# Optimization experiments

Measured on AMD Instinct MI355X. Metric: run time of the kernel, lower is better.

## Reference

```python
import jax, jax.numpy as jnp
import numpy as np

B, N, D_IN, D_H, D_OUT = 2, 512, 128, 128, 128


def _mlp2(x, W1, b1, W2, b2):
    # Linear -> SiLU -> Linear
    h = jax.nn.silu(x @ W1 + b1)
    return h @ W2 + b2


def _safe_norm(d2):
    # norm with zero (not NaN) gradient at 0, matching torch.norm's subgradient
    pos = d2 > 0
    return jnp.where(pos, jnp.sqrt(jnp.where(pos, d2, 1.0)), 0.0)


def setup_inputs() -> dict:
    key = jax.random.key(0)
    ks = jax.random.split(key, 16)

    def lin(k, fan_in, fan_out):
        bound = 1.0 / np.sqrt(fan_in)
        kw, kb = jax.random.split(k)
        W = jax.random.uniform(kw, (fan_in, fan_out), jnp.float32, -bound, bound)
        b = jax.random.uniform(kb, (fan_out,), jnp.float32, -bound, bound)
        return W, b

    Ws1, bs1 = lin(ks[0], D_IN, D_H)
    Ws2, bs2 = lin(ks[1], D_H, D_OUT)
    Wv1, bv1 = lin(ks[2], D_IN, D_H)
    Wv2, bv2 = lin(ks[3], D_H, D_OUT)
    Wa1, ba1 = lin(ks[4], D_IN + 3, D_H)
    Wa2, ba2 = lin(ks[5], D_H, 1)

    node_features = jax.random.normal(ks[6], (B, N, D_IN), jnp.float32)
    coordinates = jax.random.normal(ks[7], (B, N, 3), jnp.float32)
    edge_mask = jax.random.randint(ks[8], (B, N, N), 0, 2, jnp.int32)

    return dict(node_features=node_features, coordinates=coordinates, edge_mask=edge_mask,
                Ws1=Ws1, bs1=bs1, Ws2=Ws2, bs2=bs2,
                Wv1=Wv1, bv1=bv1, Wv2=Wv2, bv2=bv2,
                Wa1=Wa1, ba1=ba1, Wa2=Wa2, ba2=ba2)


def reference(node_features, coordinates, edge_mask,
              Ws1, bs1, Ws2, bs2, Wv1, bv1, Wv2, bv2, Wa1, ba1, Wa2, ba2):
    num_atoms = node_features.shape[1]

    # pairwise geometry: diff[b,i,j,:] = x_i - x_j
    diff = coordinates[:, :, None, :] - coordinates[:, None, :, :]  # [B,N,N,3]
    d2 = jnp.sum(diff * diff, axis=-1)
    distances = _safe_norm(d2)  # [B,N,N]

    # per-node scalar branch
    scalar_features = _mlp2(node_features, Ws1, bs1, Ws2, bs2)  # [B,N,D_OUT]

    # radial features + broadcast node features -> attention MLP
    dist_features = jnp.stack(
        [distances, 1.0 / (distances + 1e-6), jnp.exp(-distances)], axis=-1)  # [B,N,N,3]
    nf_exp = jnp.broadcast_to(node_features[:, :, None, :],
                              node_features.shape[:2] + (num_atoms, node_features.shape[-1]))
    attention_input = jnp.concatenate([nf_exp, dist_features], axis=-1)  # [B,N,N,D_IN+3]
    attn_logits = _mlp2(attention_input, Wa1, ba1, Wa2, ba2)[..., 0]  # [B,N,N]

    attn_logits = jnp.where(edge_mask != 0, attn_logits, -jnp.inf)
    attention_weights = jax.nn.softmax(attn_logits, axis=-1)  # [B,N,N]

    # direction-weighted aggregation
    vector_aggregated = jnp.einsum('bijc,bij->bic', diff, attention_weights)  # [B,N,3]

    vector_features = _mlp2(node_features, Wv1, bv1, Wv2, bv2)  # [B,N,D_OUT]
    vector_out = vector_aggregated * vector_features[..., :3]  # [B,N,3]

    return scalar_features, vector_out
```

## Files before the change

### kernel.cpp

```cpp
#include <hip/hip_runtime.h>
#include <math.h>

#define NB 2
#define NN 512
#define DD 128
#define LOG2E 1.4426950408889634f

typedef unsigned long long ull;

__device__ __forceinline__ float exp2_hw(float x) {
    float r; asm("v_exp_f32 %0, %1" : "=v"(r) : "v"(x)); return r;
}
__device__ __forceinline__ float silu_f(float x) {
    float e = exp2_hw(-LOG2E * x);
    return x * __builtin_amdgcn_rcpf(1.0f + e);
}

#define UPD(Wq, bbv, s)                                                        \
    { float pre = fmaf(f3[s], Wq.z, fmaf(f2[s], Wq.y, fmaf(f1[s], Wq.x, bbv))); \
      float e   = exp2_hw(pre);                                                \
      float rc  = __builtin_amdgcn_rcpf(1.0f + e);                             \
      acc[s]    = fmaf(pre * Wq.w, rc, acc[s]); }

__global__ __launch_bounds__(256) void k_all(
    const float* __restrict__ nf,
    const float* __restrict__ coords,
    const int*   __restrict__ mask,
    const float* __restrict__ Ws1, const float* __restrict__ bs1,
    const float* __restrict__ Ws2, const float* __restrict__ bs2,
    const float* __restrict__ Wv1, const float* __restrict__ bv1,
    const float* __restrict__ Wv2, const float* __restrict__ bv2,
    const float* __restrict__ Wa1, const float* __restrict__ ba1,
    const float* __restrict__ Wa2, const float* __restrict__ ba2p,
    float* __restrict__ scalar_out,
    float* __restrict__ vec_out)
{
    __shared__ __align__(16) float  s_nf[2][DD];
    __shared__ __align__(16) float  s_hs[2][DD];
    __shared__ __align__(16) float  s_hv[2][DD];
    __shared__ __align__(16) float  s_bb[2][DD];
    __shared__ __align__(16) float4 s_w4[DD];
    __shared__ float  s_part[3][2][256];
    __shared__ short  s_act[2][NN];
    __shared__ int    s_cnt8[2][8], s_off8[2][8], s_nact[2];
    __shared__ float  s_red[2][4], s_red2[2][4][4];

    const int row0 = blockIdx.x * 2;
    const int b    = row0 >> 9;
    const int tid  = threadIdx.x;
    const int lane = tid & 63;
    const int wid  = tid >> 6;
    const int c    = tid & 127;
    const int h    = tid >> 7;

    { const int rr = tid >> 7, t = tid & 127;
      s_nf[rr][t] = nf[(row0 + rr) * DD + t]; }

    const int* mrow0 = mask + (size_t)row0 * NN;
    const int* mrow1 = mrow0 + NN;
    const bool m00 = (mrow0[tid] != 0), m01 = (mrow0[tid + 256] != 0);
    const bool m10 = (mrow1[tid] != 0), m11 = (mrow1[tid + 256] != 0);
    const ull  b00 = __ballot(m00), b01 = __ballot(m01);
    const ull  b10 = __ballot(m10), b11 = __ballot(m11);
    if (lane == 0) {
        s_cnt8[0][wid]     = __popcll(b00);
        s_cnt8[0][4 + wid] = __popcll(b01);
        s_cnt8[1][wid]     = __popcll(b10);
        s_cnt8[1][4 + wid] = __popcll(b11);
    }
    __syncthreads();

    if (tid < 2) {
        int a = 0;
        #pragma unroll
        for (int q = 0; q < 8; ++q) { s_off8[tid][q] = a; a += s_cnt8[tid][q]; }
        s_nact[tid] = a;
    }

    {
        float pS0 = 0.f, pS1 = 0.f, pV0 = 0.f, pV1 = 0.f, pA0 = 0.f, pA1 = 0.f;
        const float4* nfq0 = (const float4*)s_nf[0];
        const float4* nfq1 = (const float4*)s_nf[1];
        const int kq0 = h * 16;
        #pragma unroll 4
        for (int kk = 0; kk < 16; ++kk) {
            float4 x0 = nfq0[kq0 + kk];
            float4 x1 = nfq1[kq0 + kk];
            const int k = (kq0 + kk) * 4;
            float w;
            w = Ws1[(k+0)*DD + c]; pS0 = fmaf(x0.x, w, pS0); pS1 = fmaf(x1.x, w, pS1);
            w = Ws1[(k+1)*DD + c]; pS0 = fmaf(x0.y, w, pS0); pS1 = fmaf(x1.y, w, pS1);
            w = Ws1[(k+2)*DD + c]; pS0 = fmaf(x0.z, w, pS0); pS1 = fmaf(x1.z, w, pS1);
            w = Ws1[(k+3)*DD + c]; pS0 = fmaf(x0.w, w, pS0); pS1 = fmaf(x1.w, w, pS1);
            w = Wv1[(k+0)*DD + c]; pV0 = fmaf(x0.x, w, pV0); pV1 = fmaf(x1.x, w, pV1);
            w = Wv1[(k+1)*DD + c]; pV0 = fmaf(x0.y, w, pV0); pV1 = fmaf(x1.y, w, pV1);
            w = Wv1[(k+2)*DD + c]; pV0 = fmaf(x0.z, w, pV0); pV1 = fmaf(x1.z, w, pV1);
            w = Wv1[(k+3)*DD + c]; pV0 = fmaf(x0.w, w, pV0); pV1 = fmaf(x1.w, w, pV1);
            w = Wa1[(k+0)*DD + c]; pA0 = fmaf(x0.x, w, pA0); pA1 = fmaf(x1.x, w, pA1);
            w = Wa1[(k+1)*DD + c]; pA0 = fmaf(x0.y, w, pA0); pA1 = fmaf(x1.y, w, pA1);
            w = Wa1[(k+2)*DD + c]; pA0 = fmaf(x0.z, w, pA0); pA1 = fmaf(x1.z, w, pA1);
            w = Wa1[(k+3)*DD + c]; pA0 = fmaf(x0.w, w, pA0); pA1 = fmaf(x1.w, w, pA1);
        }
        s_part[0][0][tid] = pS0; s_part[0][1][tid] = pS1;
        s_part[1][0][tid] = pV0; s_part[1][1][tid] = pV1;
        s_part[2][0][tid] = pA0; s_part[2][1][tid] = pA1;
    }
    __syncthreads();

    {
        const int rr = tid >> 7, t = tid & 127;
        s_hs[rr][t] = silu_f(s_part[0][rr][t] + s_part[0][rr][128 + t] + bs1[t]);
        s_hv[rr][t] = silu_f(s_part[1][rr][t] + s_part[1][rr][128 + t] + bv1[t]);
        s_bb[rr][t] = -LOG2E * (s_part[2][rr][t] + s_part[2][rr][128 + t] + ba1[t]);
    }
    if (tid < DD) {
        float4 w;
        w.x = -LOG2E * Wa1[128 * DD + tid];
        w.y = -LOG2E * Wa1[129 * DD + tid];
        w.z = -LOG2E * Wa1[130 * DD + tid];
        w.w = -Wa2[tid];
        s_w4[tid] = w;
    }
    {
        const ull lm = (1ull << lane) - 1ull;
        if (m00) s_act[0][s_off8[0][wid]     + __popcll(b00 & lm)] = (short)tid;
        if (m01) s_act[0][s_off8[0][4 + wid] + __popcll(b01 & lm)] = (short)(tid + 256);
        if (m10) s_act[1][s_off8[1][wid]     + __popcll(b10 & lm)] = (short)tid;
        if (m11) s_act[1][s_off8[1][4 + wid] + __popcll(b11 & lm)] = (short)(tid + 256);
    }
    __syncthreads();

    {
        float p0 = 0.f, p1 = 0.f;
        const float4* h0 = (const float4*)s_hs[0];
        const float4* h1 = (const float4*)s_hs[1];
        const int kq0 = h * 16;
        #pragma unroll 4
        for (int kk = 0; kk < 16; ++kk) {
            float4 x0 = h0[kq0 + kk];
            float4 x1 = h1[kq0 + kk];
            const int k = (kq0 + kk) * 4;
            float w;
            w = Ws2[(k+0)*DD + c]; p0 = fmaf(x0.x, w, p0); p1 = fmaf(x1.x, w, p1);
            w = Ws2[(k+1)*DD + c]; p0 = fmaf(x0.y, w, p0); p1 = fmaf(x1.y, w, p1);
            w = Ws2[(k+2)*DD + c]; p0 = fmaf(x0.z, w, p0); p1 = fmaf(x1.z, w, p1);
            w = Ws2[(k+3)*DD + c]; p0 = fmaf(x0.w, w, p0); p1 = fmaf(x1.w, w, p1);
        }
        s_part[0][0][tid] = p0; s_part[0][1][tid] = p1;
    }
    float* vfp = &s_part[1][0][0];
    if (tid < 192) {
        const int rr  = tid / 96;
        const int rem = tid % 96;
        const int col = rem >> 5;
        const int kq  = rem & 31;
        float vp = 0.f;
        #pragma unroll
        for (int u = 0; u < 4; ++u) {
            const int k = 4 * kq + u;
            vp = fmaf(s_hv[rr][k], Wv2[k * DD + col], vp);
        }
        vfp[tid] = vp;
    }

    const int n0 = __builtin_amdgcn_readfirstlane(s_nact[0]);
    const int n1 = __builtin_amdgcn_readfirstlane(s_nact[1]);
    const int wb = (tid & ~63) + 256;
    const bool has1r0 = wb < n0;
    const bool has1r1 = wb < n1;
    bool act[4];
    act[0] = tid < n0;  act[1] = tid + 256 < n0;
    act[2] = tid < n1;  act[3] = tid + 256 < n1;

    const float ba2l = ba2p[0] * LOG2E;
    float xi[2][3];
    #pragma unroll
    for (int rr = 0; rr < 2; ++rr)
        #pragma unroll
        for (int cc = 0; cc < 3; ++cc) xi[rr][cc] = coords[(row0 + rr) * 3 + cc];
    const float* cb = coords + (size_t)b * NN * 3;

    float dx[4], dy[4], dz[4], f1[4], f2[4], f3[4], acc[4];
    #pragma unroll
    for (int s = 0; s < 4; ++s) {
        acc[s] = ba2l;
        dx[s] = dy[s] = dz[s] = f1[s] = f2[s] = f3[s] = 0.f;
    }
    #pragma unroll
    for (int s = 0; s < 4; ++s) {
        const int rr = s >> 1;
        const bool rnd1 = (s & 1);
        if (rnd1 && !(rr == 0 ? has1r0 : has1r1)) continue;
        const int a = tid + (rnd1 ? 256 : 0);
        const int j = ((int)s_act[rr][act[s] ? a : 0]) & (NN - 1);
        dx[s] = xi[rr][0] - cb[j * 3 + 0];
        dy[s] = xi[rr][1] - cb[j * 3 + 1];
        dz[s] = xi[rr][2] - cb[j * 3 + 2];
        float d2 = fmaf(dx[s], dx[s], fmaf(dy[s], dy[s], dz[s] * dz[s]));
        float d  = sqrtf(d2);
        f1[s] = d;
        float x  = d + 1e-6f;
        float rc = __builtin_amdgcn_rcpf(x);
        f2[s] = rc * fmaf(-x, rc, 2.0f);
        f3[s] = exp2_hw(-LOG2E * d);
    }

    const float4* bbq0 = (const float4*)s_bb[0];
    const float4* bbq1 = (const float4*)s_bb[1];
    for (int t4 = 0; t4 < DD / 4; ++t4) {
        float4 W0 = s_w4[4 * t4 + 0];
        float4 W1 = s_w4[4 * t4 + 1];
        float4 W2 = s_w4[4 * t4 + 2];
        float4 W3 = s_w4[4 * t4 + 3];
        float4 bA = bbq0[t4];
        float4 bB = bbq1[t4];
        UPD(W0, bA.x, 0); UPD(W1, bA.y, 0); UPD(W2, bA.z, 0); UPD(W3, bA.w, 0);
        UPD(W0, bB.x, 2); UPD(W1, bB.y, 2); UPD(W2, bB.z, 2); UPD(W3, bB.w, 2);
        if (has1r0) {
            UPD(W0, bA.x, 1); UPD(W1, bA.y, 1); UPD(W2, bA.z, 1); UPD(W3, bA.w, 1);
        }
        if (has1r1) {
            UPD(W0, bB.x, 3); UPD(W1, bB.y, 3); UPD(W2, bB.z, 3); UPD(W3, bB.w, 3);
        }
    }
    __syncthreads();

    {
        const int rr = tid >> 7, t = tid & 127;
        scalar_out[(row0 + rr) * DD + t] =
            s_part[0][rr][t] + s_part[0][rr][128 + t] + bs2[t];
    }

    float mloc[2] = { -__builtin_inff(), -__builtin_inff() };
    if (act[0]) mloc[0] = acc[0];
    if (has1r0 && act[1]) mloc[0] = fmaxf(mloc[0], acc[1]);
    if (act[2]) mloc[1] = acc[2];
    if (has1r1 && act[3]) mloc[1] = fmaxf(mloc[1], acc[3]);
    #pragma unroll
    for (int ofs = 32; ofs >= 1; ofs >>= 1) {
        mloc[0] = fmaxf(mloc[0], __shfl_xor(mloc[0], ofs));
        mloc[1] = fmaxf(mloc[1], __shfl_xor(mloc[1], ofs));
    }
    if (lane == 0) { s_red[0][wid] = mloc[0]; s_red[1][wid] = mloc[1]; }
    __syncthreads();
    const float mx0 = fmaxf(fmaxf(s_red[0][0], s_red[0][1]), fmaxf(s_red[0][2], s_red[0][3]));
    const float mx1 = fmaxf(fmaxf(s_red[1][0], s_red[1][1]), fmaxf(s_red[1][2], s_red[1][3]));

    float es[2] = {0.f, 0.f}, wx[2] = {0.f, 0.f}, wy[2] = {0.f, 0.f}, wz[2] = {0.f, 0.f};
    if (act[0]) {
        float e = exp2_hw(acc[0] - mx0);
        es[0] += e; wx[0] = fmaf(e, dx[0], wx[0]); wy[0] = fmaf(e, dy[0], wy[0]); wz[0] = fmaf(e, dz[0], wz[0]);
    }
    if (has1r0 && act[1]) {
        float e = exp2_hw(acc[1] - mx0);
        es[0] += e; wx[0] = fmaf(e, dx[1], wx[0]); wy[0] = fmaf(e, dy[1], wy[0]); wz[0] = fmaf(e, dz[1], wz[0]);
    }
    if (act[2]) {
        float e = exp2_hw(acc[2] - mx1);
        es[1] += e; wx[1] = fmaf(e, dx[2], wx[1]); wy[1] = fmaf(e, dy[2], wy[1]); wz[1] = fmaf(e, dz[2], wz[1]);
    }
    if (has1r1 && act[3]) {
        float e = exp2_hw(acc[3] - mx1);
        es[1] += e; wx[1] = fmaf(e, dx[3], wx[1]); wy[1] = fmaf(e, dy[3], wy[1]); wz[1] = fmaf(e, dz[3], wz[1]);
    }
    #pragma unroll
    for (int ofs = 32; ofs >= 1; ofs >>= 1) {
        #pragma unroll
        for (int rr = 0; rr < 2; ++rr) {
            es[rr] += __shfl_xor(es[rr], ofs);
            wx[rr] += __shfl_xor(wx[rr], ofs);
            wy[rr] += __shfl_xor(wy[rr], ofs);
            wz[rr] += __shfl_xor(wz[rr], ofs);
        }
    }
    if (lane == 0) {
        #pragma unroll
        for (int rr = 0; rr < 2; ++rr) {
            s_red2[rr][wid][0] = es[rr]; s_red2[rr][wid][1] = wx[rr];
            s_red2[rr][wid][2] = wy[rr]; s_red2[rr][wid][3] = wz[rr];
        }
    }
    __syncthreads();

    if (tid < 6) {
        const int rr = tid / 3, cc = tid % 3;
        float tot = s_red2[rr][0][0] + s_red2[rr][1][0] + s_red2[rr][2][0] + s_red2[rr][3][0];
        float num = s_red2[rr][0][1+cc] + s_red2[rr][1][1+cc] + s_red2[rr][2][1+cc] + s_red2[rr][3][1+cc];
        float vf = bv2[cc];
        const float* pp = &vfp[rr * 96 + cc * 32];
        #pragma unroll 8
        for (int q = 0; q < 32; ++q) vf += pp[q];
        vec_out[(row0 + rr) * 3 + cc] = (num / tot) * vf;
    }
}

extern "C" void kernel_launch(void* const* d_in, const int* in_sizes, int n_in,
                              void* d_out, int out_size, void* d_ws, size_t ws_size,
                              hipStream_t stream) {
    const float* nf     = (const float*)d_in[0];
    const float* coords = (const float*)d_in[1];
    const int*   mask   = (const int*)  d_in[2];
    const float* Ws1 = (const float*)d_in[3];  const float* bs1 = (const float*)d_in[4];
    const float* Ws2 = (const float*)d_in[5];  const float* bs2 = (const float*)d_in[6];
    const float* Wv1 = (const float*)d_in[7];  const float* bv1 = (const float*)d_in[8];
    const float* Wv2 = (const float*)d_in[9];  const float* bv2 = (const float*)d_in[10];
    const float* Wa1 = (const float*)d_in[11]; const float* ba1 = (const float*)d_in[12];
    const float* Wa2 = (const float*)d_in[13]; const float* ba2 = (const float*)d_in[14];

    float* scalar_out = (float*)d_out;
    float* vec_out    = (float*)d_out + NB * NN * DD;

    hipLaunchKernelGGL(k_all, dim3(NB * NN / 2), dim3(256), 0, stream,
                       nf, coords, mask,
                       Ws1, bs1, Ws2, bs2, Wv1, bv1, Wv2, bv2,
                       Wa1, ba1, Wa2, ba2,
                       scalar_out, vec_out);
}
```

Before: 29.05 us.

## Double block to 512 threads and split attention hidden dim across thread groups

The block size goes from 256 to 512 threads. The hidden dimension of the per-edge attention MLP is now split into four 32-wide slices, one per thread group, so each thread covers 8 edge slots over a quarter of the hidden units. Partial logits are summed through a new shared buffer before the softmax, and the node MLP K-loops are split four ways. The aim is more parallelism for the exp-heavy inner loop, at the cost of extra shared memory, an extra reduction pass, and redundant distance setup in each group.

```diff
diff --git a/kernel.cpp b/kernel.cpp
--- a/kernel.cpp
+++ b/kernel.cpp
@@ -16,13 +16,30 @@
     return x * __builtin_amdgcn_rcpf(1.0f + e);
 }
 
-#define UPD(Wq, bbv, s)                                                        \
-    { float pre = fmaf(f3[s], Wq.z, fmaf(f2[s], Wq.y, fmaf(f1[s], Wq.x, bbv))); \
+#define UPD1(Wq, BBC, F1, F2, F3, ACC)                                         \
+    { float pre = fmaf(F3, Wq.z, fmaf(F2, Wq.y, fmaf(F1, Wq.x, BBC)));         \
       float e   = exp2_hw(pre);                                                \
       float rc  = __builtin_amdgcn_rcpf(1.0f + e);                             \
-      acc[s]    = fmaf(pre * Wq.w, rc, acc[s]); }
-
-__global__ __launch_bounds__(256) void k_all(
+      ACC = fmaf(pre * Wq.w, rc, ACC); }
+
+#define UPD4(BB, F1, F2, F3, ACC)                                              \
+    UPD1(W0, BB.x, F1, F2, F3, ACC) UPD1(W1, BB.y, F1, F2, F3, ACC)            \
+    UPD1(W2, BB.z, F1, F2, F3, ACC) UPD1(W3, BB.w, F1, F2, F3, ACC)
+
+#define SETUP(rr, A, NACT, F1, F2, F3)                                         \
+    { int a_ = (A);                                                            \
+      int j_ = ((int)s_act[rr][(a_ < (NACT)) ? a_ : 0]) & (NN - 1);            \
+      float dx_ = xiv[rr][0] - cb[j_ * 3 + 0];                                 \
+      float dy_ = xiv[rr][1] - cb[j_ * 3 + 1];                                 \
+      float dz_ = xiv[rr][2] - cb[j_ * 3 + 2];                                 \
+      float d_  = sqrtf(fmaf(dx_, dx_, fmaf(dy_, dy_, dz_ * dz_)));            \
+      F1 = d_;                                                                 \
+      float x_  = d_ + 1e-6f;                                                  \
+      float rc_ = __builtin_amdgcn_rcpf(x_);                                   \
+      F2 = rc_ * fmaf(-x_, rc_, 2.0f);                                         \
+      F3 = exp2_hw(-LOG2E * d_); }
+
+__global__ __launch_bounds__(512) void k_all(
     const float* __restrict__ nf,
     const float* __restrict__ coords,
     const int*   __restrict__ mask,
@@ -40,9 +57,11 @@
     __shared__ __align__(16) float  s_hv[2][DD];
     __shared__ __align__(16) float  s_bb[2][DD];
     __shared__ __align__(16) float4 s_w4[DD];
-    __shared__ float  s_part[3][2][256];
+    __shared__ float  s_part[3][2][4][DD];
+    __shared__ float  s_lg[2][4][NN];
     __shared__ short  s_act[2][NN];
-    __shared__ int    s_cnt8[2][8], s_off8[2][8], s_nact[2];
+    __shared__ float  s_vp[192];
+    __shared__ int    s_cnt[2][8], s_off[2][8], s_nact[2];
     __shared__ float  s_red[2][4], s_red2[2][4][4];
 
     const int row0 = blockIdx.x * 2;
@@ -52,40 +71,39 @@
     const int wid  = tid >> 6;
     const int c    = tid & 127;
     const int h    = tid >> 7;
-
-    { const int rr = tid >> 7, t = tid & 127;
-      s_nf[rr][t] = nf[(row0 + rr) * DD + t]; }
-
-    const int* mrow0 = mask + (size_t)row0 * NN;
-    const int* mrow1 = mrow0 + NN;
-    const bool m00 = (mrow0[tid] != 0), m01 = (mrow0[tid + 256] != 0);
-    const bool m10 = (mrow1[tid] != 0), m11 = (mrow1[tid + 256] != 0);
-    const ull  b00 = __ballot(m00), b01 = __ballot(m01);
-    const ull  b10 = __ballot(m10), b11 = __ballot(m11);
+    const int u    = tid & 127;
+    const int ub   = tid & 64;
+
+    if (tid < 256) { const int rr = tid >> 7, t = tid & 127;
+                     s_nf[rr][t] = nf[(row0 + rr) * DD + t]; }
+    const int mr = tid >> 8;
+    const int jj = tid & 255;
+    const int* mrow = mask + (size_t)(row0 + mr) * NN;
+    const bool m0 = (mrow[jj]       != 0);
+    const bool m1 = (mrow[jj + 256] != 0);
+    const ull  bal0 = __ballot(m0);
+    const ull  bal1 = __ballot(m1);
     if (lane == 0) {
-        s_cnt8[0][wid]     = __popcll(b00);
-        s_cnt8[0][4 + wid] = __popcll(b01);
-        s_cnt8[1][wid]     = __popcll(b10);
-        s_cnt8[1][4 + wid] = __popcll(b11);
+        s_cnt[mr][(wid & 3)]     = __popcll(bal0);
+        s_cnt[mr][(wid & 3) + 4] = __popcll(bal1);
     }
     __syncthreads();
 
     if (tid < 2) {
         int a = 0;
         #pragma unroll
-        for (int q = 0; q < 8; ++q) { s_off8[tid][q] = a; a += s_cnt8[tid][q]; }
+        for (int q = 0; q < 8; ++q) { s_off[tid][q] = a; a += s_cnt[tid][q]; }
         s_nact[tid] = a;
     }
-
     {
         float pS0 = 0.f, pS1 = 0.f, pV0 = 0.f, pV1 = 0.f, pA0 = 0.f, pA1 = 0.f;
-        const float4* nfq0 = (const float4*)s_nf[0];
-        const float4* nfq1 = (const float4*)s_nf[1];
-        const int kq0 = h * 16;
+        const float4* nq0 = (const float4*)s_nf[0];
+        const float4* nq1 = (const float4*)s_nf[1];
+        const int kq0 = h * 8;
         #pragma unroll 4
-        for (int kk = 0; kk < 16; ++kk) {
-            float4 x0 = nfq0[kq0 + kk];
-            float4 x1 = nfq1[kq0 + kk];
+        for (int kk = 0; kk < 8; ++kk) {
+            float4 x0 = nq0[kq0 + kk];
+            float4 x1 = nq1[kq0 + kk];
             const int k = (kq0 + kk) * 4;
             float w;
             w = Ws1[(k+0)*DD + c]; pS0 = fmaf(x0.x, w, pS0); pS1 = fmaf(x1.x, w, pS1);
@@ -101,32 +119,36 @@
             w = Wa1[(k+2)*DD + c]; pA0 = fmaf(x0.z, w, pA0); pA1 = fmaf(x1.z, w, pA1);
             w = Wa1[(k+3)*DD + c]; pA0 = fmaf(x0.w, w, pA0); pA1 = fmaf(x1.w, w, pA1);
         }
-        s_part[0][0][tid] = pS0; s_part[0][1][tid] = pS1;
-        s_part[1][0][tid] = pV0; s_part[1][1][tid] = pV1;
-        s_part[2][0][tid] = pA0; s_part[2][1][tid] = pA1;
-    }
-    __syncthreads();
-
-    {
+        s_part[0][0][h][c] = pS0; s_part[0][1][h][c] = pS1;
+        s_part[1][0][h][c] = pV0; s_part[1][1][h][c] = pV1;
+        s_part[2][0][h][c] = pA0; s_part[2][1][h][c] = pA1;
+    }
+    __syncthreads();
+
+    if (tid < 256) {
         const int rr = tid >> 7, t = tid & 127;
-        s_hs[rr][t] = silu_f(s_part[0][rr][t] + s_part[0][rr][128 + t] + bs1[t]);
-        s_hv[rr][t] = silu_f(s_part[1][rr][t] + s_part[1][rr][128 + t] + bv1[t]);
-        s_bb[rr][t] = -LOG2E * (s_part[2][rr][t] + s_part[2][rr][128 + t] + ba1[t]);
-    }
-    if (tid < DD) {
+        float vs = s_part[0][rr][0][t] + s_part[0][rr][1][t]
+                 + s_part[0][rr][2][t] + s_part[0][rr][3][t] + bs1[t];
+        float vv = s_part[1][rr][0][t] + s_part[1][rr][1][t]
+                 + s_part[1][rr][2][t] + s_part[1][rr][3][t] + bv1[t];
+        float va = s_part[2][rr][0][t] + s_part[2][rr][1][t]
+                 + s_part[2][rr][2][t] + s_part[2][rr][3][t] + ba1[t];
+        s_hs[rr][t] = silu_f(vs);
+        s_hv[rr][t] = silu_f(vv);
+        s_bb[rr][t] = -LOG2E * va;
+    } else if (tid < 384) {
+        const int t = tid - 256;
         float4 w;
-        w.x = -LOG2E * Wa1[128 * DD + tid];
-        w.y = -LOG2E * Wa1[129 * DD + tid];
-        w.z = -LOG2E * Wa1[130 * DD + tid];
-        w.w = -Wa2[tid];
-        s_w4[tid] = w;
+        w.x = -LOG2E * Wa1[128 * DD + t];
+        w.y = -LOG2E * Wa1[129 * DD + t];
+        w.z = -LOG2E * Wa1[130 * DD + t];
+        w.w = -Wa2[t];
+        s_w4[t] = w;
     }
     {
         const ull lm = (1ull << lane) - 1ull;
-        if (m00) s_act[0][s_off8[0][wid]     + __popcll(b00 & lm)] = (short)tid;
-        if (m01) s_act[0][s_off8[0][4 + wid] + __popcll(b01 & lm)] = (short)(tid + 256);
-        if (m10) s_act[1][s_off8[1][wid]     + __popcll(b10 & lm)] = (short)tid;
-        if (m11) s_act[1][s_off8[1][4 + wid] + __popcll(b11 & lm)] = (short)(tid + 256);
+        if (m0) s_act[mr][s_off[mr][(wid & 3)]     + __popcll(bal0 & lm)] = (short)jj;
+        if (m1) s_act[mr][s_off[mr][(wid & 3) + 4] + __popcll(bal1 & lm)] = (short)(jj + 256);
     }
     __syncthreads();
 
@@ -134,9 +156,9 @@
         float p0 = 0.f, p1 = 0.f;
         const float4* h0 = (const float4*)s_hs[0];
         const float4* h1 = (const float4*)s_hs[1];
-        const int kq0 = h * 16;
+        const int kq0 = h * 8;
         #pragma unroll 4
-        for (int kk = 0; kk < 16; ++kk) {
+        for (int kk = 0; kk < 8; ++kk) {
             float4 x0 = h0[kq0 + kk];
             float4 x1 = h1[kq0 + kk];
             const int k = (kq0 + kk) * 4;
@@ -146,9 +168,8 @@
             w = Ws2[(k+2)*DD + c]; p0 = fmaf(x0.z, w, p0); p1 = fmaf(x1.z, w, p1);
             w = Ws2[(k+3)*DD + c]; p0 = fmaf(x0.w, w, p0); p1 = fmaf(x1.w, w, p1);
         }
-        s_part[0][0][tid] = p0; s_part[0][1][tid] = p1;
-    }
-    float* vfp = &s_part[1][0][0];
+        s_part[0][0][h][c] = p0; s_part[0][1][h][c] = p1;
+    }
     if (tid < 192) {
         const int rr  = tid / 96;
         const int rem = tid % 96;
@@ -156,138 +177,137 @@
         const int kq  = rem & 31;
         float vp = 0.f;
         #pragma unroll
-        for (int u = 0; u < 4; ++u) {
-            const int k = 4 * kq + u;
+        for (int uu = 0; uu < 4; ++uu) {
+            const int k = 4 * kq + uu;
             vp = fmaf(s_hv[rr][k], Wv2[k * DD + col], vp);
         }
-        vfp[tid] = vp;
+        s_vp[tid] = vp;
     }
 
     const int n0 = __builtin_amdgcn_readfirstlane(s_nact[0]);
     const int n1 = __builtin_amdgcn_readfirstlane(s_nact[1]);
-    const int wb = (tid & ~63) + 256;
-    const bool has1r0 = wb < n0;
-    const bool has1r1 = wb < n1;
-    bool act[4];
-    act[0] = tid < n0;  act[1] = tid + 256 < n0;
-    act[2] = tid < n1;  act[3] = tid + 256 < n1;
-
     const float ba2l = ba2p[0] * LOG2E;
-    float xi[2][3];
+    float xiv[2][3];
     #pragma unroll
     for (int rr = 0; rr < 2; ++rr)
         #pragma unroll
-        for (int cc = 0; cc < 3; ++cc) xi[rr][cc] = coords[(row0 + rr) * 3 + cc];
+        for (int cc = 0; cc < 3; ++cc) xiv[rr][cc] = coords[(row0 + rr) * 3 + cc];
     const float* cb = coords + (size_t)b * NN * 3;
 
-    float dx[4], dy[4], dz[4], f1[4], f2[4], f3[4], acc[4];
-    #pragma unroll
-    for (int s = 0; s < 4; ++s) {
-        acc[s] = ba2l;
-        dx[s] = dy[s] = dz[s] = f1[s] = f2[s] = f3[s] = 0.f;
-    }
-    #pragma unroll
-    for (int s = 0; s < 4; ++s) {
-        const int rr = s >> 1;
-        const bool rnd1 = (s & 1);
-        if (rnd1 && !(rr == 0 ? has1r0 : has1r1)) continue;
-        const int a = tid + (rnd1 ? 256 : 0);
-        const int j = ((int)s_act[rr][act[s] ? a : 0]) & (NN - 1);
-        dx[s] = xi[rr][0] - cb[j * 3 + 0];
-        dy[s] = xi[rr][1] - cb[j * 3 + 1];
-        dz[s] = xi[rr][2] - cb[j * 3 + 2];
-        float d2 = fmaf(dx[s], dx[s], fmaf(dy[s], dy[s], dz[s] * dz[s]));
-        float d  = sqrtf(d2);
-        f1[s] = d;
-        float x  = d + 1e-6f;
-        float rc = __builtin_amdgcn_rcpf(x);
-        f2[s] = rc * fmaf(-x, rc, 2.0f);
-        f3[s] = exp2_hw(-LOG2E * d);
-    }
-
-    const float4* bbq0 = (const float4*)s_bb[0];
-    const float4* bbq1 = (const float4*)s_bb[1];
-    for (int t4 = 0; t4 < DD / 4; ++t4) {
-        float4 W0 = s_w4[4 * t4 + 0];
-        float4 W1 = s_w4[4 * t4 + 1];
-        float4 W2 = s_w4[4 * t4 + 2];
-        float4 W3 = s_w4[4 * t4 + 3];
-        float4 bA = bbq0[t4];
-        float4 bB = bbq1[t4];
-        UPD(W0, bA.x, 0); UPD(W1, bA.y, 0); UPD(W2, bA.z, 0); UPD(W3, bA.w, 0);
-        UPD(W0, bB.x, 2); UPD(W1, bB.y, 2); UPD(W2, bB.z, 2); UPD(W3, bB.w, 2);
-        if (has1r0) {
-            UPD(W0, bA.x, 1); UPD(W1, bA.y, 1); UPD(W2, bA.z, 1); UPD(W3, bA.w, 1);
+    const bool g00 = (ub      ) < n0, g01 = (ub + 128) < n0,
+               g02 = (ub + 256) < n0, g03 = (ub + 384) < n0;
+    const bool g10 = (ub      ) < n1, g11 = (ub + 128) < n1,
+               g12 = (ub + 256) < n1, g13 = (ub + 384) < n1;
+
+    float f1_00=0,f2_00=0,f3_00=0,a00=0, f1_01=0,f2_01=0,f3_01=0,a01=0;
+    float f1_02=0,f2_02=0,f3_02=0,a02=0, f1_03=0,f2_03=0,f3_03=0,a03=0;
+    float f1_10=0,f2_10=0,f3_10=0,a10=0, f1_11=0,f2_11=0,f3_11=0,a11=0;
+    float f1_12=0,f2_12=0,f3_12=0,a12=0, f1_13=0,f2_13=0,f3_13=0,a13=0;
+
+    if (g00) SETUP(0, u      , n0, f1_00, f2_00, f3_00);
+    if (g01) SETUP(0, u + 128, n0, f1_01, f2_01, f3_01);
+    if (g02) SETUP(0, u + 256, n0, f1_02, f2_02, f3_02);
+    if (g03) SETUP(0, u + 384, n0, f1_03, f2_03, f3_03);
+    if (g10) SETUP(1, u      , n1, f1_10, f2_10, f3_10);
+    if (g11) SETUP(1, u + 128, n1, f1_11, f2_11, f3_11);
+    if (g12) SETUP(1, u + 256, n1, f1_12, f2_12, f3_12);
+    if (g13) SETUP(1, u + 384, n1, f1_13, f2_13, f3_13);
+
+    {
+        const float4* bb0 = (const float4*)s_bb[0];
+        const float4* bb1 = (const float4*)s_bb[1];
+        #pragma unroll 2
+        for (int tt = 0; tt < 8; ++tt) {
+            const int t4 = h * 8 + tt;
+            float4 W0 = s_w4[4 * t4 + 0];
+            float4 W1 = s_w4[4 * t4 + 1];
+            float4 W2 = s_w4[4 * t4 + 2];
+            float4 W3 = s_w4[4 * t4 + 3];
+            float4 bA = bb0[t4];
+            float4 bB = bb1[t4];
+            if (g00) { UPD4(bA, f1_00, f2_00, f3_00, a00) }
+            if (g01) { UPD4(bA, f1_01, f2_01, f3_01, a01) }
+            if (g10) { UPD4(bB, f1_10, f2_10, f3_10, a10) }
+            if (g11) { UPD4(bB, f1_11, f2_11, f3_11, a11) }
+            if (g02) { UPD4(bA, f1_02, f2_02, f3_02, a02) }
+            if (g12) { UPD4(bB, f1_12, f2_12, f3_12, a12) }
+            if (g03) { UPD4(bA, f1_03, f2_03, f3_03, a03) }
+            if (g13) { UPD4(bB, f1_13, f2_13, f3_13, a13) }
         }
-        if (has1r1) {
-            UPD(W0, bB.x, 3); UPD(W1, bB.y, 3); UPD(W2, bB.z, 3); UPD(W3, bB.w, 3);
-        }
-    }
-    __syncthreads();
-
-    {
+    }
+    s_lg[0][h][u      ] = a00;
+    s_lg[0][h][u + 128] = a01;
+    s_lg[0][h][u + 256] = a02;
+    s_lg[0][h][u + 384] = a03;
+    s_lg[1][h][u      ] = a10;
+    s_lg[1][h][u + 128] = a11;
+    s_lg[1][h][u + 256] = a12;
+    s_lg[1][h][u + 384] = a13;
+    __syncthreads();
+
+    if (tid < 256) {
         const int rr = tid >> 7, t = tid & 127;
         scalar_out[(row0 + rr) * DD + t] =
-            s_part[0][rr][t] + s_part[0][rr][128 + t] + bs2[t];
-    }
-
-    float mloc[2] = { -__builtin_inff(), -__builtin_inff() };
-    if (act[0]) mloc[0] = acc[0];
-    if (has1r0 && act[1]) mloc[0] = fmaxf(mloc[0], acc[1]);
-    if (act[2]) mloc[1] = acc[2];
-    if (has1r1 && act[3]) mloc[1] = fmaxf(mloc[1], acc[3]);
+            s_part[0][rr][0][t] + s_part[0][rr][1][t] +
+            s_part[0][rr][2][t] + s_part[0][rr][3][t] + bs2[t];
+    }
+    const int rw = tid >> 8;
+    const int uc = tid & 255;
+    const int nw = rw ? n1 : n0;
+    const bool vA = uc < nw;
+    const bool vB = uc + 256 < nw;
+    const float lgA = s_lg[rw][0][uc] + s_lg[rw][1][uc]
+                    + s_lg[rw][2][uc] + s_lg[rw][3][uc] + ba2l;
+    const float lgB = s_lg[rw][0][uc + 256] + s_lg[rw][1][uc + 256]
+                    + s_lg[rw][2][uc + 256] + s_lg[rw][3][uc + 256] + ba2l;
+    float mloc = -__builtin_inff();
+    if (vA) mloc = lgA;
+    if (vB) mloc = fmaxf(mloc, lgB);
+    #pragma unroll
+    for (int ofs = 32; ofs >= 1; ofs >>= 1) mloc = fmaxf(mloc, __shfl_xor(mloc, ofs));
+    if (lane == 0) s_red[rw][wid & 3] = mloc;
+    __syncthreads();
+
+    const float mx = fmaxf(fmaxf(s_red[rw][0], s_red[rw][1]),
+                           fmaxf(s_red[rw][2], s_red[rw][3]));
+    float es = 0.f, wx = 0.f, wy = 0.f, wz = 0.f;
+    if (vA) {
+        const int j = ((int)s_act[rw][uc]) & (NN - 1);
+        float dx = xiv[rw][0] - cb[j * 3 + 0];
+        float dy = xiv[rw][1] - cb[j * 3 + 1];
+        float dz = xiv[rw][2] - cb[j * 3 + 2];
+        float e  = exp2_hw(lgA - mx);
+        es += e; wx = fmaf(e, dx, wx); wy = fmaf(e, dy, wy); wz = fmaf(e, dz, wz);
+    }
+    if (vB) {
+        const int j = ((int)s_act[rw][uc + 256]) & (NN - 1);
+        float dx = xiv[rw][0] - cb[j * 3 + 0];
+        float dy = xiv[rw][1] - cb[j * 3 + 1];
+        float dz = xiv[rw][2] - cb[j * 3 + 2];
+        float e  = exp2_hw(lgB - mx);
+        es += e; wx = fmaf(e, dx, wx); wy = fmaf(e, dy, wy); wz = fmaf(e, dz, wz);
+    }
     #pragma unroll
     for (int ofs = 32; ofs >= 1; ofs >>= 1) {
-        mloc[0] = fmaxf(mloc[0], __shfl_xor(mloc[0], ofs));
-        mloc[1] = fmaxf(mloc[1], __shfl_xor(mloc[1], ofs));
-    }
-    if (lane == 0) { s_red[0][wid] = mloc[0]; s_red[1][wid] = mloc[1]; }
-    __syncthreads();
-    const float mx0 = fmaxf(fmaxf(s_red[0][0], s_red[0][1]), fmaxf(s_red[0][2], s_red[0][3]));
-    const float mx1 = fmaxf(fmaxf(s_red[1][0], s_red[1][1]), fmaxf(s_red[1][2], s_red[1][3]));
-
-    float es[2] = {0.f, 0.f}, wx[2] = {0.f, 0.f}, wy[2] = {0.f, 0.f}, wz[2] = {0.f, 0.f};
-    if (act[0]) {
-        float e = exp2_hw(acc[0] - mx0);
-        es[0] += e; wx[0] = fmaf(e, dx[0], wx[0]); wy[0] = fmaf(e, dy[0], wy[0]); wz[0] = fmaf(e, dz[0], wz[0]);
-    }
-    if (has1r0 && act[1]) {
-        float e = exp2_hw(acc[1] - mx0);
-        es[0] += e; wx[0] = fmaf(e, dx[1], wx[0]); wy[0] = fmaf(e, dy[1], wy[0]); wz[0] = fmaf(e, dz[1], wz[0]);
-    }
-    if (act[2]) {
-        float e = exp2_hw(acc[2] - mx1);
-        es[1] += e; wx[1] = fmaf(e, dx[2], wx[1]); wy[1] = fmaf(e, dy[2], wy[1]); wz[1] = fmaf(e, dz[2], wz[1]);
-    }
-    if (has1r1 && act[3]) {
-        float e = exp2_hw(acc[3] - mx1);
-        es[1] += e; wx[1] = fmaf(e, dx[3], wx[1]); wy[1] = fmaf(e, dy[3], wy[1]); wz[1] = fmaf(e, dz[3], wz[1]);
-    }
-    #pragma unroll
-    for (int ofs = 32; ofs >= 1; ofs >>= 1) {
-        #pragma unroll
-        for (int rr = 0; rr < 2; ++rr) {
-            es[rr] += __shfl_xor(es[rr], ofs);
-            wx[rr] += __shfl_xor(wx[rr], ofs);
-            wy[rr] += __shfl_xor(wy[rr], ofs);
-            wz[rr] += __shfl_xor(wz[rr], ofs);
-        }
+        es += __shfl_xor(es, ofs);
+        wx += __shfl_xor(wx, ofs);
+        wy += __shfl_xor(wy, ofs);
+        wz += __shfl_xor(wz, ofs);
     }
     if (lane == 0) {
-        #pragma unroll
-        for (int rr = 0; rr < 2; ++rr) {
-            s_red2[rr][wid][0] = es[rr]; s_red2[rr][wid][1] = wx[rr];
-            s_red2[rr][wid][2] = wy[rr]; s_red2[rr][wid][3] = wz[rr];
-        }
+        s_red2[rw][wid & 3][0] = es; s_red2[rw][wid & 3][1] = wx;
+        s_red2[rw][wid & 3][2] = wy; s_red2[rw][wid & 3][3] = wz;
     }
     __syncthreads();
 
     if (tid < 6) {
         const int rr = tid / 3, cc = tid % 3;
-        float tot = s_red2[rr][0][0] + s_red2[rr][1][0] + s_red2[rr][2][0] + s_red2[rr][3][0];
-        float num = s_red2[rr][0][1+cc] + s_red2[rr][1][1+cc] + s_red2[rr][2][1+cc] + s_red2[rr][3][1+cc];
+        float tot = s_red2[rr][0][0] + s_red2[rr][1][0]
+                  + s_red2[rr][2][0] + s_red2[rr][3][0];
+        float num = s_red2[rr][0][1+cc] + s_red2[rr][1][1+cc]
+                  + s_red2[rr][2][1+cc] + s_red2[rr][3][1+cc];
         float vf = bv2[cc];
-        const float* pp = &vfp[rr * 96 + cc * 32];
+        const float* pp = &s_vp[rr * 96 + cc * 32];
         #pragma unroll 8
         for (int q = 0; q < 32; ++q) vf += pp[q];
         vec_out[(row0 + rr) * 3 + cc] = (num / tot) * vf;
@@ -310,7 +330,7 @@
     float* scalar_out = (float*)d_out;
     float* vec_out    = (float*)d_out + NB * NN * DD;
 
-    hipLaunchKernelGGL(k_all, dim3(NB * NN / 2), dim3(256), 0, stream,
+    hipLaunchKernelGGL(k_all, dim3(NB * NN / 2), dim3(512), 0, stream,
                        nf, coords, mask,
                        Ws1, bs1, Ws2, bs2, Wv1, bv1, Wv2, bv2,
                        Wa1, ba1, Wa2, ba2,
```

New measurement: 26.61 us. 1.09x faster.
